# Optimization experiments

Hardware: AMD Instinct MI355X
Metric: run time of the kernel (lower is better)

The kernel has to match this reference:

```python
import jax, jax.numpy as jnp
import numpy as np

ALPHA, GAMMA, Q = 0.602, 0.101, 8.0  # spsa defaults; func(x)=x0^2+Q*x1^2
INIT_VAL = 0.01


def _func(x):
    # x: (..., 2)
    return x[..., 0] ** 2 + Q * x[..., 1] ** 2


def setup_inputs() -> dict:
    key = jax.random.key(0)
    k1, k2 = jax.random.split(key)
    num_itr, bs, npar = 1000, 16384, 2
    X0 = jax.random.uniform(k1, (bs, npar), dtype=jnp.float32)  # scaled to [-10,10] in reference
    a = INIT_VAL * jnp.ones((num_itr,), jnp.float32)
    c = INIT_VAL * jnp.ones((num_itr,), jnp.float32)
    # Rademacher bits: delta = 2*bit - 1 in {-1,+1}
    delta_bits = jax.random.randint(k2, (num_itr, bs, npar), 0, 2, dtype=jnp.int32)
    return {"X0": X0, "a": a, "c": c, "delta_bits": delta_bits, "num_itr": num_itr}


def reference(X0, a, c, delta_bits, num_itr):
    x0 = X0 * 20.0 - 10.0  # torch.rand(bs,Npar)*20-10
    A = int(np.floor(0.1 * num_itr))
    k = jnp.arange(1, num_itr + 1, dtype=jnp.float32)  # iteration index k = 1..maxiter
    ck = c / (k + 1.0) ** GAMMA                 # (n,) per-step perturbation size
    ak = a / (k + 1.0 + A) ** ALPHA             # (n,) per-step learning rate
    delta = (2 * delta_bits - 1).astype(jnp.float32)  # (n, bs, p) Rademacher

    def step(x, inp):
        ck_k, ak_k, d = inp                     # scalar, scalar, (bs, p)
        xp = x + ck_k * d
        xm = x - ck_k * d
        # graditer=1: ghat = (f(xp)-f(xm)) / (2*ck*delta), broadcast over params
        ghat = (_func(xp) - _func(xm))[..., None] / (2.0 * ck_k * d)
        return x - ak_k * ghat, None

    x_final, _ = jax.lax.scan(step, x0, (ck, ak, delta))
    return x_final
```

## Files before the change

### kernel.cpp

```cpp
#include <hip/hip_runtime.h>
#include <math.h>


#define SEGLEN 64
#define NSEG   16
#define NTAB   (NSEG * SEGLEN)
#define BLKT   512

__global__ __launch_bounds__(BLKT) void spsa_fused(
    const float2* __restrict__ X0,
    const int2*   __restrict__ bits,
    const float*  __restrict__ a_arr,
    float2*       __restrict__ out,
    int n, int bs, int A)
{
    __shared__ float s_nw[NTAB];
    __shared__ float s_m0[NSEG][64], s_m1[NSEG][64],
                     s_m2[NSEG][64], s_m3[NSEG][64];

    const int tid  = threadIdx.x;
    const int lane = tid & 63;
    const int wave = tid >> 6;
    const int b    = blockIdx.x * 64 + lane;
    const int kmax = n - 1;

    const int segA = wave * 2;
    const int segB = wave * 2 + 1;
    const int kA   = segA * SEGLEN;
    const int kB   = segB * SEGLEN;
    const int2* p  = bits + b;

    int2 v[SEGLEN];
    #pragma unroll
    for (int j = 0; j < SEGLEN; ++j) {
        int k = kA + j;
        k = (k > kmax) ? kmax : k;
        v[j] = p[(size_t)k * bs];
    }

    #pragma unroll
    for (int t = 0; t < 2; ++t) {
        const int k = tid * 2 + t;
        float nw = 0.0f;
        if (k < n) nw = -2.0f * a_arr[k] / powf((float)(k + 2 + A), 0.602f);
        s_nw[k] = nw;
    }
    __syncthreads();

    auto stepm = [](int2 d, float nw, float& m00, float& m01,
                    float& m10, float& m11) {
        unsigned sb = ((unsigned)(d.x ^ d.y)) << 31;
        float qs  = __uint_as_float(0x41000000u ^ sb);
        float nws = __uint_as_float(__float_as_uint(nw) ^ sb);
        float u0 = fmaf(qs, m10, m00);
        float u1 = fmaf(qs, m11, m01);
        m00 = fmaf(nw,  u0, m00);
        m01 = fmaf(nw,  u1, m01);
        m10 = fmaf(nws, u0, m10);
        m11 = fmaf(nws, u1, m11);
    };

    float a00 = 1.f, a01 = 0.f, a10 = 0.f, a11 = 1.f;
    #pragma unroll
    for (int j = 0; j < SEGLEN; ++j) stepm(v[j], s_nw[kA + j], a00, a01, a10, a11);

    #pragma unroll
    for (int j = 0; j < SEGLEN; ++j) {
        int k = kB + j;
        k = (k > kmax) ? kmax : k;
        v[j] = p[(size_t)k * bs];
    }
    float b00 = 1.f, b01 = 0.f, b10 = 0.f, b11 = 1.f;
    #pragma unroll
    for (int j = 0; j < SEGLEN; ++j) stepm(v[j], s_nw[kB + j], b00, b01, b10, b11);

    s_m0[segA][lane] = a00; s_m1[segA][lane] = a01;
    s_m2[segA][lane] = a10; s_m3[segA][lane] = a11;
    s_m0[segB][lane] = b00; s_m1[segB][lane] = b01;
    s_m2[segB][lane] = b10; s_m3[segB][lane] = b11;

    const int pair = tid >> 6;
    #pragma unroll
    for (int lvl = 0; lvl < 4; ++lvl) {
        const int str = 1 << lvl;
        const int h   = 8 >> lvl;
        __syncthreads();
        if (pair < h) {
            const int pos = (pair * 2) * str;
            float L0 = s_m0[pos][lane],       L1 = s_m1[pos][lane];
            float L2 = s_m2[pos][lane],       L3 = s_m3[pos][lane];
            float R0 = s_m0[pos + str][lane], R1 = s_m1[pos + str][lane];
            float R2 = s_m2[pos + str][lane], R3 = s_m3[pos + str][lane];
            s_m0[pos][lane] = fmaf(R0, L0, R1 * L2);
            s_m1[pos][lane] = fmaf(R0, L1, R1 * L3);
            s_m2[pos][lane] = fmaf(R2, L0, R3 * L2);
            s_m3[pos][lane] = fmaf(R2, L1, R3 * L3);
        }
    }
    __syncthreads();

    if (tid < 64 && b < bs) {
        float M0 = s_m0[0][lane], M1 = s_m1[0][lane];
        float M2 = s_m2[0][lane], M3 = s_m3[0][lane];
        float2 xin = X0[b];
        float v0 = xin.x * 20.0f - 10.0f;
        float v1 = xin.y * 20.0f - 10.0f;
        float r0 = fmaf(M0, v0, M1 * v1);
        float r1 = fmaf(M2, v0, M3 * v1);
        out[b] = make_float2(r0, r1);
    }
}

__global__ void spsa_fallback(
    const float2* __restrict__ X0, const int2* __restrict__ bits,
    const float* __restrict__ a_arr, float2* __restrict__ out,
    int n, int bs, int A)
{
    int b = blockIdx.x * 256 + threadIdx.x;
    if (b >= bs) return;
    float2 xin = X0[b];
    float x0 = xin.x * 20.0f - 10.0f;
    float x1 = xin.y * 20.0f - 10.0f;
    for (int k = 0; k < n; ++k) {
        float nw = -2.0f * a_arr[k] / powf((float)(k + 2 + A), 0.602f);
        int2 d = bits[(size_t)k * bs + b];
        unsigned sb = ((unsigned)(d.x ^ d.y)) << 31;
        float qs  = __uint_as_float(0x41000000u ^ sb);
        float nws = __uint_as_float(__float_as_uint(nw) ^ sb);
        float u = fmaf(qs, x1, x0);
        x0 = fmaf(nw,  u, x0);
        x1 = fmaf(nws, u, x1);
    }
    out[b] = make_float2(x0, x1);
}

extern "C" void kernel_launch(void* const* d_in, const int* in_sizes, int n_in,
                              void* d_out, int out_size, void* d_ws, size_t ws_size,
                              hipStream_t stream) {
    const float2* X0   = (const float2*)d_in[0];
    const float*  a    = (const float*) d_in[1];
    const int2*   bits = (const int2*)  d_in[3];
    float2*       out  = (float2*)d_out;

    const int bs = in_sizes[0] / 2;
    const int n  = in_sizes[1];
    const int A  = (int)floor(0.1 * (double)n);

    if (n <= NTAB && (bs % 64) == 0) {
        spsa_fused<<<bs / 64, BLKT, 0, stream>>>(X0, bits, a, out, n, bs, A);
    } else {
        const int grid = (bs + 255) / 256;
        spsa_fallback<<<grid, 256, 0, stream>>>(X0, bits, a, out, n, bs, A);
    }
}
```

Before: 27.85 us.

## Use one segment per wave with 1024 threads and software-pipelined bit loads

```diff
diff --git a/kernel.cpp b/kernel.cpp
--- a/kernel.cpp
+++ b/kernel.cpp
@@ -4,8 +4,10 @@
 
 #define SEGLEN 64
 #define NSEG   16
+#define PH     4
+#define PHL    16
 #define NTAB   (NSEG * SEGLEN)
-#define BLKT   512
+#define BLKT   1024
 
 __global__ __launch_bounds__(BLKT) void spsa_fused(
     const float2* __restrict__ X0,
@@ -23,27 +25,21 @@
     const int wave = tid >> 6;
     const int b    = blockIdx.x * 64 + lane;
     const int kmax = n - 1;
-
-    const int segA = wave * 2;
-    const int segB = wave * 2 + 1;
-    const int kA   = segA * SEGLEN;
-    const int kB   = segB * SEGLEN;
+    const int k0   = wave * SEGLEN;
     const int2* p  = bits + b;
 
-    int2 v[SEGLEN];
+    int2 v[PHL];
     #pragma unroll
-    for (int j = 0; j < SEGLEN; ++j) {
-        int k = kA + j;
+    for (int j = 0; j < PHL; ++j) {
+        int k = k0 + j;
         k = (k > kmax) ? kmax : k;
         v[j] = p[(size_t)k * bs];
     }
 
-    #pragma unroll
-    for (int t = 0; t < 2; ++t) {
-        const int k = tid * 2 + t;
+    {
         float nw = 0.0f;
-        if (k < n) nw = -2.0f * a_arr[k] / powf((float)(k + 2 + A), 0.602f);
-        s_nw[k] = nw;
+        if (tid < n) nw = -2.0f * a_arr[tid] / powf((float)(tid + 2 + A), 0.602f);
+        s_nw[tid] = nw;
     }
     __syncthreads();
 
@@ -60,26 +56,24 @@
         m11 = fmaf(nws, u1, m11);
     };
 
-    float a00 = 1.f, a01 = 0.f, a10 = 0.f, a11 = 1.f;
+    float m00 = 1.f, m01 = 0.f, m10 = 0.f, m11 = 1.f;
     #pragma unroll
-    for (int j = 0; j < SEGLEN; ++j) stepm(v[j], s_nw[kA + j], a00, a01, a10, a11);
+    for (int ph = 0; ph < PH; ++ph) {
+        #pragma unroll
+        for (int j = 0; j < PHL; ++j) {
+            stepm(v[j], s_nw[k0 + ph * PHL + j], m00, m01, m10, m11);
+            if (ph + 1 < PH) {
+                int k = k0 + (ph + 1) * PHL + j;
+                k = (k > kmax) ? kmax : k;
+                v[j] = p[(size_t)k * bs];
+            }
+        }
+    }
 
-    #pragma unroll
-    for (int j = 0; j < SEGLEN; ++j) {
-        int k = kB + j;
-        k = (k > kmax) ? kmax : k;
-        v[j] = p[(size_t)k * bs];
-    }
-    float b00 = 1.f, b01 = 0.f, b10 = 0.f, b11 = 1.f;
-    #pragma unroll
-    for (int j = 0; j < SEGLEN; ++j) stepm(v[j], s_nw[kB + j], b00, b01, b10, b11);
+    s_m0[wave][lane] = m00; s_m1[wave][lane] = m01;
+    s_m2[wave][lane] = m10; s_m3[wave][lane] = m11;
 
-    s_m0[segA][lane] = a00; s_m1[segA][lane] = a01;
-    s_m2[segA][lane] = a10; s_m3[segA][lane] = a11;
-    s_m0[segB][lane] = b00; s_m1[segB][lane] = b01;
-    s_m2[segB][lane] = b10; s_m3[segB][lane] = b11;
-
-    const int pair = tid >> 6;
+    const int pair = wave;
     #pragma unroll
     for (int lvl = 0; lvl < 4; ++lvl) {
         const int str = 1 << lvl;
```

Measured after the change: 25.31 us. 9.1% less time.
